# Kernel tuning notes

Measured on AMD Instinct MI355X. Metric: run time of the kernel, lower is better.

The kernel has to match this reference:

```python
import jax, jax.numpy as jnp
import numpy as np

N_NODES = 10000
N_EDGES = 160000
MUL = 128            # channel multiplicity of node features
N_ELEM = 10          # node_attrs scalars (num elements)
N_EDGE_FEATS = 8     # radial basis size
W_NUMEL = 4 * MUL    # 4 uvu paths, 128 weights each
AVG_NEIGH = 16.0
INV_SQRT3 = 0.5773502691896258  # CG coefficient for 1o x 1o -> 0e (dot product path)


def setup_inputs() -> dict:
    key = jax.random.key(0)
    ks = jax.random.split(key, 12)
    node_attrs = jax.random.uniform(ks[0], (N_NODES, N_ELEM), dtype=jnp.float32)
    node_feats = jax.random.normal(ks[1], (N_NODES, MUL * 4), dtype=jnp.float32)  # 128x0e + 128x1o flattened
    edge_attrs = jax.random.normal(ks[2], (N_EDGES, 4), dtype=jnp.float32)        # Y0 (1) + Y1 (3)
    edge_feats = jax.random.normal(ks[3], (N_EDGES, N_EDGE_FEATS), dtype=jnp.float32)
    edge_index = jax.random.randint(ks[4], (2, N_EDGES), 0, N_NODES, dtype=jnp.int64)
    # learned parameters (xavier-ish scales; e3nn path norms folded into weights)
    W_up0 = jax.random.normal(ks[5], (MUL, MUL), dtype=jnp.float32) / np.sqrt(MUL)
    W_up1 = jax.random.normal(ks[6], (MUL, MUL), dtype=jnp.float32) / np.sqrt(MUL)
    W_tpw = jax.random.normal(ks[7], (N_ELEM, N_EDGE_FEATS, W_NUMEL), dtype=jnp.float32) / np.sqrt(N_ELEM * N_EDGE_FEATS)
    W_lin0 = jax.random.normal(ks[8], (2 * MUL, MUL), dtype=jnp.float32) / np.sqrt(2 * MUL)
    W_lin1 = jax.random.normal(ks[9], (2 * MUL, MUL), dtype=jnp.float32) / np.sqrt(2 * MUL)
    W_sk0 = jax.random.normal(ks[10], (MUL, N_ELEM, MUL), dtype=jnp.float32) / np.sqrt(MUL * N_ELEM)
    W_sk1 = jax.random.normal(ks[11], (MUL, N_ELEM, MUL), dtype=jnp.float32) / np.sqrt(MUL * N_ELEM)
    return dict(node_attrs=node_attrs, node_feats=node_feats, edge_attrs=edge_attrs,
                edge_feats=edge_feats, edge_index=edge_index,
                W_up0=W_up0, W_up1=W_up1, W_tpw=W_tpw,
                W_lin0=W_lin0, W_lin1=W_lin1, W_sk0=W_sk0, W_sk1=W_sk1)


def reference(node_attrs, node_feats, edge_attrs, edge_feats, edge_index,
              W_up0, W_up1, W_tpw, W_lin0, W_lin1, W_sk0, W_sk1):
    N = node_feats.shape[0]
    sender, receiver = edge_index[0], edge_index[1]
    x0 = node_feats[:, :MUL]                       # [N,128] scalars (0e)
    x1 = node_feats[:, MUL:].reshape(N, MUL, 3)    # [N,128,3] vectors (1o)

    # skip_tp: FullyConnectedTensorProduct(node_feats, node_attrs -> 128x0e+128x1o)
    sc0 = jnp.einsum('nu,na,uak->nk', x0, node_attrs, W_sk0)        # [N,128]
    sc1 = jnp.einsum('num,na,uak->nkm', x1, node_attrs, W_sk1)      # [N,128,3]

    # linear_up: per-l linear
    h0 = x0 @ W_up0                                   # [N,128]
    h1 = jnp.einsum('num,uk->nkm', x1, W_up1)         # [N,128,3]

    # per-edge TP weights: einsum('be,ba,aek->bk')
    tpw = jnp.einsum('be,ba,aek->bk', edge_feats, node_attrs[sender], W_tpw)  # [E,512]
    w1, w2, w3, w4 = tpw[:, :MUL], tpw[:, MUL:2*MUL], tpw[:, 2*MUL:3*MUL], tpw[:, 3*MUL:]

    Y0 = edge_attrs[:, 0]       # [E]
    Y1 = edge_attrs[:, 1:4]     # [E,3]
    hs0 = h0[sender]            # [E,128] gather
    hs1 = h1[sender]            # [E,128,3]

    # conv_tp (uvu, external per-edge weights), 4 CG paths:
    m0a = w1 * hs0 * Y0[:, None]                                       # 0e x 0e -> 0e
    m1a = (w2 * hs0)[:, :, None] * Y1[:, None, :]                      # 0e x 1o -> 1o
    m1b = hs1 * (w3 * Y0[:, None])[:, :, None]                         # 1o x 0e -> 1o
    m0b = w4 * (INV_SQRT3 * jnp.einsum('eum,em->eu', hs1, Y1))         # 1o x 1o -> 0e
    m0 = jnp.concatenate([m0a, m0b], axis=1)    # [E,256]  irreps_mid 0e block
    m1 = jnp.concatenate([m1a, m1b], axis=1)    # [E,256,3] irreps_mid 1o block

    # scatter_sum over receiver
    msg0 = jax.ops.segment_sum(m0, receiver, num_segments=N)   # [N,256]
    msg1 = jax.ops.segment_sum(m1, receiver, num_segments=N)   # [N,256,3]

    # linear (irreps_mid -> 128x0e+128x1o) / avg_num_neighbors + skip
    out0 = (msg0 @ W_lin0) / AVG_NEIGH + sc0                        # [N,128]
    out1 = jnp.einsum('num,uk->nkm', msg1, W_lin1) / AVG_NEIGH + sc1  # [N,128,3]
    return jnp.concatenate([out0, out1.reshape(N, MUL * 3)], axis=1)  # [N,512]
```

## Files before the change

### kernel.cpp

```cpp
#include <hip/hip_runtime.h>

#define NN 10000
#define NE 160000
#define NBK0 157
#define NBK1 469

constexpr float INV_AVG = 1.0f / 16.0f;
constexpr float INV_SQRT3F = 0.5773502691896258f;

typedef __attribute__((ext_vector_type(8))) short short8v;
typedef __attribute__((ext_vector_type(8))) unsigned short ushort8v;
typedef __attribute__((ext_vector_type(4))) float float4v;

#define OF_UP0 0
#define OF_UP1 16384
#define OF_SK0 32768
#define OF_SK1 196608
#define OF_LN0 360448
#define OF_LN1 393216
#define WPK_TOT 425984
#define WTP_TOT 49152

__device__ __forceinline__ unsigned short f2bf(float f) {
    unsigned int u = __float_as_uint(f);
    return (unsigned short)((u + 0x7FFFu + ((u >> 16) & 1u)) >> 16);
}
__device__ __forceinline__ float bf2f(unsigned short h) {
    return __uint_as_float(((unsigned int)h) << 16);
}

__global__ __launch_bounds__(256) void prep_w_kernel(
    const float* __restrict__ W_up0, const float* __restrict__ W_up1,
    const float* __restrict__ W_sk0, const float* __restrict__ W_sk1,
    const float* __restrict__ W_lin0, const float* __restrict__ W_lin1,
    unsigned short* __restrict__ wpk)
{
    const int g = blockIdx.x * 256 + threadIdx.x;
    if (g >= WPK_TOT / 8) return;
    const float* src; int local, base; bool sk = false;
    if (g < 2048)       { src = W_up0;  local = g;         base = OF_UP0; }
    else if (g < 4096)  { src = W_up1;  local = g - 2048;  base = OF_UP1; }
    else if (g < 24576) { src = W_sk0;  local = g - 4096;  base = OF_SK0; sk = true; }
    else if (g < 45056) { src = W_sk1;  local = g - 24576; base = OF_SK1; sk = true; }
    else if (g < 49152) { src = W_lin0; local = g - 45056; base = OF_LN0; }
    else                { src = W_lin1; local = g - 49152; base = OF_LN1; }
    const int k8 = local >> 7, n = local & 127;
    ushort8v v;
    #pragma unroll
    for (int j = 0; j < 8; ++j) {
        const int k = k8 * 8 + j;
        int row;
        if (sk) { const int a = k >> 7, u = k & 127; row = u * 10 + a; }
        else    { row = k; }
        v[j] = f2bf(src[(size_t)row * 128 + n]);
    }
    *(ushort8v*)(wpk + (size_t)base + (size_t)local * 8) = v;
}

__global__ __launch_bounds__(256) void prep_wt_kernel(
    const float* __restrict__ W_tpw, unsigned short* __restrict__ wtp)
{
    const int g = blockIdx.x * 256 + threadIdx.x;
    if (g >= 6144) return;
    const int k8 = g >> 9, col = g & 511;
    ushort8v v;
    #pragma unroll
    for (int j = 0; j < 8; ++j) {
        const int k = k8 * 8 + j;
        v[j] = (k < 80) ? f2bf(W_tpw[(size_t)k * 512 + col]) : (unsigned short)0;
    }
    *(ushort8v*)(wtp + (size_t)g * 8) = v;
}

__global__ __launch_bounds__(256, 2) void node_mfma_kernel(
    const float* __restrict__ node_attrs,
    const float* __restrict__ node_feats,
    const unsigned short* __restrict__ wpk,
    float* __restrict__ hbuf,
    float* __restrict__ out)
{
    __shared__ __align__(16) unsigned short habuf[1024][8];
    __shared__ __align__(16) unsigned short bbuf[2][1024][8];
    __shared__ float atrow[64][10];

    const int t = threadIdx.x;
    const int bid = blockIdx.x;
    const bool m1 = (bid >= NBK0);
    const int r0 = m1 ? (bid - NBK0) * 64 : bid * 64;
    const int RTOT = m1 ? 30000 : 10000;

    const unsigned short* __restrict__ wup = wpk + (m1 ? OF_UP1 : OF_UP0);
    const unsigned short* __restrict__ wsk = wpk + (m1 ? OF_SK1 : OF_SK0);

    const int rg_ = t >> 2, pg_ = t & 3;
    const int rr_g = min(r0 + rg_, RTOT - 1);
    int n_g, m_g;
    if (!m1) { n_g = rr_g; m_g = 0; }
    else     { n_g = rr_g / 3; m_g = rr_g - n_g * 3; }
    const int wq = rg_ >> 4, rlq = rg_ & 15;

    #pragma unroll
    for (int q = 0; q < 4; ++q) {
        const int sl = pg_ * 4 + q, ss = sl >> 2, kb = sl & 3;
        const int k0 = ss * 32 + kb * 8;
        ushort8v v;
        if (!m1) {
            const float4 xa_ = *(const float4*)(node_feats + (size_t)n_g * 512 + k0);
            const float4 xb_ = *(const float4*)(node_feats + (size_t)n_g * 512 + k0 + 4);
            v[0] = f2bf(xa_.x); v[1] = f2bf(xa_.y); v[2] = f2bf(xa_.z); v[3] = f2bf(xa_.w);
            v[4] = f2bf(xb_.x); v[5] = f2bf(xb_.y); v[6] = f2bf(xb_.z); v[7] = f2bf(xb_.w);
        } else {
            #pragma unroll
            for (int j = 0; j < 8; ++j)
                v[j] = f2bf(node_feats[(size_t)n_g * 512 + 128 + (k0 + j) * 3 + m_g]);
        }
        *(ushort8v*)&habuf[((ss * 4 + wq) * 4 + kb) * 16 + rlq][0] = v;
    }
    for (int i = t; i < 640; i += 256) {
        const int r = i / 10, a = i - r * 10;
        const int rr = min(r0 + r, RTOT - 1);
        const int n = m1 ? (rr / 3) : rr;
        atrow[r][a] = node_attrs[n * 10 + a];
    }
    __syncthreads();

    const int w = t >> 6, lane = t & 63;
    const int rl = lane & 15, kq = lane >> 4;

    {
        float4v hacc[8];
        #pragma unroll
        for (int nt = 0; nt < 8; ++nt) hacc[nt] = (float4v){0.f, 0.f, 0.f, 0.f};

        #pragma unroll
        for (int ss = 0; ss < 4; ++ss) {
            const short8v af = *(const short8v*)&habuf[((ss * 4 + w) * 4 + kq) * 16 + rl][0];
            #pragma unroll
            for (int nt = 0; nt < 8; ++nt) {
                const short8v bf = *(const short8v*)(wup +
                    ((size_t)((ss * 4 + kq) * 128 + nt * 16 + rl)) * 8);
                hacc[nt] = __builtin_amdgcn_mfma_f32_16x16x32_bf16(af, bf, hacc[nt], 0, 0, 0);
            }
        }
        #pragma unroll
        for (int nt = 0; nt < 8; ++nt)
            #pragma unroll
            for (int v2 = 0; v2 < 4; ++v2) {
                const int rr = r0 + w * 16 + kq * 4 + v2;
                if (rr < RTOT) {
                    const int col = nt * 16 + rl;
                    if (!m1) hbuf[(size_t)rr * 512 + col] = hacc[nt][v2];
                    else {
                        const int n = rr / 3, m = rr - n * 3;
                        hbuf[(size_t)n * 512 + 128 + m * 128 + col] = hacc[nt][v2];
                    }
                }
            }
    }

    float4v sacc[8];
    #pragma unroll
    for (int nt = 0; nt < 8; ++nt) sacc[nt] = (float4v){0.f, 0.f, 0.f, 0.f};

    #pragma unroll
    for (int i = 0; i < 4; ++i) {
        const int s = i * 256 + t;
        const int ssb = s >> 9, ntb = (s >> 6) & 7, kbb = (s >> 4) & 3, nlb = s & 15;
        const int k8 = ssb * 4 + kbb;
        const int n = ntb * 16 + nlb;
        *(ushort8v*)&bbuf[0][s][0] =
            *(const ushort8v*)(wsk + ((size_t)(k8 * 128 + n)) * 8);
    }
    __syncthreads();

    int cur = 0;
    for (int ks = 0; ks < 20; ++ks) {
        ushort8v tmp[4];
        if (ks < 19) {
            #pragma unroll
            for (int i = 0; i < 4; ++i) {
                const int s = i * 256 + t;
                const int ssb = s >> 9, ntb = (s >> 6) & 7, kbb = (s >> 4) & 3, nlb = s & 15;
                const int k8 = (ks + 1) * 8 + ssb * 4 + kbb;
                const int n = ntb * 16 + nlb;
                tmp[i] = *(const ushort8v*)(wsk + ((size_t)(k8 * 128 + n)) * 8);
            }
        }

        short8v af[2];
        #pragma unroll
        for (int ss = 0; ss < 2; ++ss) {
            const int kp = ks * 64 + ss * 32 + kq * 8;
            const int a = kp >> 7, u0 = kp & 127;
            const ushort8v xh = *(const ushort8v*)&habuf[
                (((u0 >> 5) * 4 + w) * 4 + ((u0 >> 3) & 3)) * 16 + rl][0];
            const float av = atrow[w * 16 + rl][a];
            ushort8v vv;
            #pragma unroll
            for (int j = 0; j < 8; ++j) vv[j] = f2bf(bf2f(xh[j]) * av);
            af[ss] = (short8v)vv;
        }

        #pragma unroll
        for (int ss = 0; ss < 2; ++ss)
            #pragma unroll
            for (int nt = 0; nt < 8; ++nt) {
                const short8v bf =
                    *(const short8v*)&bbuf[cur][((ss * 8 + nt) * 4 + kq) * 16 + rl][0];
                sacc[nt] = __builtin_amdgcn_mfma_f32_16x16x32_bf16(af[ss], bf, sacc[nt], 0, 0, 0);
            }

        if (ks < 19) {
            #pragma unroll
            for (int i = 0; i < 4; ++i) {
                const int s = i * 256 + t;
                *(ushort8v*)&bbuf[cur ^ 1][s][0] = tmp[i];
            }
        }
        __syncthreads();
        cur ^= 1;
    }

    #pragma unroll
    for (int nt = 0; nt < 8; ++nt)
        #pragma unroll
        for (int v2 = 0; v2 < 4; ++v2) {
            const int rr = r0 + w * 16 + kq * 4 + v2;
            if (rr < RTOT) {
                const int col = nt * 16 + rl;
                if (!m1) out[(size_t)rr * 512 + col] = sacc[nt][v2];
                else {
                    const int n = rr / 3, m = rr - n * 3;
                    out[(size_t)n * 512 + 128 + col * 3 + m] = sacc[nt][v2];
                }
            }
        }
}

__global__ __launch_bounds__(256) void hist_kernel(
    const int* __restrict__ recv, int* __restrict__ cnt)
{
    const int e = blockIdx.x * 256 + threadIdx.x;
    if (e < NE) atomicAdd(&cnt[recv[e]], 1);
}

__global__ __launch_bounds__(256) void scan_kernel(
    const int* __restrict__ cnt, int* __restrict__ row_start,
    int* __restrict__ head)
{
    __shared__ int part[256];
    const int t = threadIdx.x;
    const int base = t * 40;
    int s = 0;
    if (base < NN)
        for (int b = 0; b < 40; ++b) s += cnt[base + b];
    part[t] = s;
    __syncthreads();
    const int local = s;
    for (int off = 1; off < 256; off <<= 1) {
        const int v = (t >= off) ? part[t - off] : 0;
        __syncthreads();
        part[t] += v;
        __syncthreads();
    }
    const int excl = part[t] - local;
    if (base < NN) {
        int run = excl;
        for (int b = 0; b < 40; ++b) {
            row_start[base + b] = run;
            head[base + b] = run;
            run += cnt[base + b];
        }
    }
    if (t == 0) row_start[NN] = NE;
}

__global__ __launch_bounds__(256) void scatter_kernel(
    const int* __restrict__ recv, int* __restrict__ head,
    int* __restrict__ elist)
{
    const int e = blockIdx.x * 256 + threadIdx.x;
    if (e < NE) {
        const int p = atomicAdd(&head[recv[e]], 1);
        elist[p] = e;
    }
}

__global__ __launch_bounds__(256) void pack2_kernel(
    const float* __restrict__ node_attrs,
    const float* __restrict__ edge_attrs,
    const float* __restrict__ edge_feats,
    const int*  __restrict__ edge_index,
    const int*  __restrict__ elist,
    unsigned short* __restrict__ zpk,
    float* __restrict__ ypk)
{
    const int pos = blockIdx.x * 256 + threadIdx.x;
    if (pos >= NE) return;
    const int e = elist[pos];
    const int snd = edge_index[e];

    float ef[8];
    *(float4*)&ef[0] = *(const float4*)(edge_feats + (size_t)e * 8);
    *(float4*)&ef[4] = *(const float4*)(edge_feats + (size_t)e * 8 + 4);
    float at[10];
    #pragma unroll
    for (int a = 0; a < 10; ++a) at[a] = node_attrs[(size_t)snd * 10 + a];

    #pragma unroll
    for (int k8 = 0; k8 < 12; ++k8) {
        ushort8v v;
        #pragma unroll
        for (int j = 0; j < 8; ++j) {
            const int A = k8 * 8 + j;
            const float z = (A < 80) ? at[A >> 3] * ef[A & 7] : 0.f;
            v[j] = f2bf(z);
        }
        *(ushort8v*)(zpk + ((size_t)k8 * NE + pos) * 8) = v;
    }

    const float4 ea = *(const float4*)(edge_attrs + (size_t)e * 4);
    *(float4*)(ypk + (size_t)pos * 8) = ea;
    *(float4*)(ypk + (size_t)pos * 8 + 4) =
        make_float4(__int_as_float(snd), 0.f, 0.f, 0.f);
}

__global__ __launch_bounds__(512, 2) void gather_mfma_kernel(
    const unsigned short* __restrict__ wtp,
    const float* __restrict__ hbuf,
    const int*  __restrict__ row_start,
    const unsigned short* __restrict__ zpk,
    const float* __restrict__ ypk,
    float* __restrict__ msgbuf)
{
    __shared__ __align__(16) unsigned short zb[384][8];
    __shared__ float yb[32][9];

    const int t = threadIdx.x;
    const int ngrp = blockIdx.x;
    const int w8 = t >> 6, lane = t & 63;
    const int p = w8 >> 2;
    const int w = w8 & 3;
    const int rl = lane & 15, kq = lane >> 4;

    short8v breg[2][3][2];
    #pragma unroll
    for (int wi = 0; wi < 2; ++wi)
        #pragma unroll
        for (int ks = 0; ks < 3; ++ks)
            #pragma unroll
            for (int ct = 0; ct < 2; ++ct) {
                const int col = p * 256 + wi * 128 + w * 32 + ct * 16 + rl;
                breg[wi][ks][ct] = *(const short8v*)(wtp +
                    ((size_t)((ks * 4 + kq) * 512 + col)) * 8);
            }

    for (int nn = 0; nn < 4; ++nn) {
        const int node = ngrp * 4 + nn;
        const int rowst = row_start[node];
        const int deg = row_start[node + 1] - rowst;

        float nacc[2][4];
        #pragma unroll
        for (int ct = 0; ct < 2; ++ct)
            #pragma unroll
            for (int j = 0; j < 4; ++j) nacc[ct][j] = 0.f;

        for (int ce = 0; ce < deg; ce += 32) {
            const int cl = min(32, deg - ce);
            __syncthreads();

            if (t < 384) {
                const int s = t;
                const int rl2 = s & 15, kq2 = (s >> 4) & 3;
                const int rowt2 = (s >> 6) & 1, ks2 = s >> 7;
                const int e = rowt2 * 16 + rl2;
                const int k8 = ks2 * 4 + kq2;
                ushort8v v = {0, 0, 0, 0, 0, 0, 0, 0};
                if (e < cl)
                    v = *(const ushort8v*)(zpk + ((size_t)k8 * NE + rowst + ce + e) * 8);
                *(ushort8v*)&zb[s][0] = v;
            }
            else if (t >= 448) {
                const int tt = t - 448;
                const int row = tt >> 1, half = tt & 1;
                float4 v = make_float4(0.f, 0.f, 0.f, 0.f);
                if (row < cl)
                    v = *(const float4*)(ypk + (size_t)(rowst + ce + row) * 8 + half * 4);
                yb[row][half * 4 + 0] = v.x;
                yb[row][half * 4 + 1] = v.y;
                yb[row][half * 4 + 2] = v.z;
                yb[row][half * 4 + 3] = v.w;
            }
            __syncthreads();

            if (p == 0) {
                #pragma unroll
                for (int rt = 0; rt < 2; ++rt) {
                    if (rt == 1 && cl <= 16) continue;
                    float h0v[4][2];
                    #pragma unroll
                    for (int v = 0; v < 4; ++v) {
                        const int e = rt * 16 + kq * 4 + v;
                        const int snd = __float_as_int(yb[e][4]);
                        const float* hrow = hbuf + (size_t)snd * 512;
                        #pragma unroll
                        for (int ct = 0; ct < 2; ++ct)
                            h0v[v][ct] = hrow[w * 32 + ct * 16 + rl];
                    }
                    float4v acc[2][2];
                    #pragma unroll
                    for (int wi = 0; wi < 2; ++wi)
                        #pragma unroll
                        for (int ct = 0; ct < 2; ++ct)
                            acc[wi][ct] = (float4v){0.f, 0.f, 0.f, 0.f};
                    #pragma unroll
                    for (int ks = 0; ks < 3; ++ks) {
                        const short8v af =
                            *(const short8v*)&zb[ks * 128 + rt * 64 + lane][0];
                        #pragma unroll
                        for (int wi = 0; wi < 2; ++wi)
                            #pragma unroll
                            for (int ct = 0; ct < 2; ++ct)
                                acc[wi][ct] = __builtin_amdgcn_mfma_f32_16x16x32_bf16(
                                    af, breg[wi][ks][ct], acc[wi][ct], 0, 0, 0);
                    }
                    #pragma unroll
                    for (int v = 0; v < 4; ++v) {
                        const int e = rt * 16 + kq * 4 + v;
                        const float Y0  = yb[e][0];
                        const float Y10 = yb[e][1];
                        const float Y11 = yb[e][2];
                        const float Y12 = yb[e][3];
                        #pragma unroll
                        for (int ct = 0; ct < 2; ++ct) {
                            const float tA = acc[0][ct][v];
                            const float tB = acc[1][ct][v];
                            const float h0 = h0v[v][ct];
                            nacc[ct][0] = fmaf(tA * Y0, h0, nacc[ct][0]);
                            const float tm = tB * h0;
                            nacc[ct][1] = fmaf(tm, Y10, nacc[ct][1]);
                            nacc[ct][2] = fmaf(tm, Y11, nacc[ct][2]);
                            nacc[ct][3] = fmaf(tm, Y12, nacc[ct][3]);
                        }
                    }
                }
            } else {
                #pragma unroll
                for (int rt = 0; rt < 2; ++rt) {
                    if (rt == 1 && cl <= 16) continue;
                    float hA[4][2], hB[4][2], hC[4][2];
                    #pragma unroll
                    for (int v = 0; v < 4; ++v) {
                        const int e = rt * 16 + kq * 4 + v;
                        const int snd = __float_as_int(yb[e][4]);
                        const float* hrow = hbuf + (size_t)snd * 512;
                        #pragma unroll
                        for (int ct = 0; ct < 2; ++ct) {
                            const int c = w * 32 + ct * 16 + rl;
                            hA[v][ct] = hrow[128 + c];
                            hB[v][ct] = hrow[256 + c];
                            hC[v][ct] = hrow[384 + c];
                        }
                    }
                    float4v acc[2][2];
                    #pragma unroll
                    for (int wi = 0; wi < 2; ++wi)
                        #pragma unroll
                        for (int ct = 0; ct < 2; ++ct)
                            acc[wi][ct] = (float4v){0.f, 0.f, 0.f, 0.f};
                    #pragma unroll
                    for (int ks = 0; ks < 3; ++ks) {
                        const short8v af =
                            *(const short8v*)&zb[ks * 128 + rt * 64 + lane][0];
                        #pragma unroll
                        for (int wi = 0; wi < 2; ++wi)
                            #pragma unroll
                            for (int ct = 0; ct < 2; ++ct)
                                acc[wi][ct] = __builtin_amdgcn_mfma_f32_16x16x32_bf16(
                                    af, breg[wi][ks][ct], acc[wi][ct], 0, 0, 0);
                    }
                    #pragma unroll
                    for (int v = 0; v < 4; ++v) {
                        const int e = rt * 16 + kq * 4 + v;
                        const float Y0  = yb[e][0];
                        const float Y10 = yb[e][1];
                        const float Y11 = yb[e][2];
                        const float Y12 = yb[e][3];
                        #pragma unroll
                        for (int ct = 0; ct < 2; ++ct) {
                            const float tA = acc[0][ct][v];
                            const float tB = acc[1][ct][v];
                            const float t2 = tA * Y0;
                            nacc[ct][1] = fmaf(t2, hA[v][ct], nacc[ct][1]);
                            nacc[ct][2] = fmaf(t2, hB[v][ct], nacc[ct][2]);
                            nacc[ct][3] = fmaf(t2, hC[v][ct], nacc[ct][3]);
                            float d = hA[v][ct] * Y10;
                            d = fmaf(hB[v][ct], Y11, d);
                            d = fmaf(hC[v][ct], Y12, d);
                            nacc[ct][0] = fmaf(tB * INV_SQRT3F, d, nacc[ct][0]);
                        }
                    }
                }
            }
        }

        float red[2][4];
        #pragma unroll
        for (int ct = 0; ct < 2; ++ct)
            #pragma unroll
            for (int j = 0; j < 4; ++j) {
                float v = nacc[ct][j];
                v += __shfl_xor(v, 16, 64);
                v += __shfl_xor(v, 32, 64);
                red[ct][j] = v;
            }
        if (kq == 0) {
            float* mrow = msgbuf + (size_t)node * 1024;
            #pragma unroll
            for (int ct = 0; ct < 2; ++ct) {
                const int c = w * 32 + ct * 16 + rl;
                if (p == 0) {
                    mrow[c]       = red[ct][0];
                    mrow[256 + c] = red[ct][1];
                    mrow[512 + c] = red[ct][2];
                    mrow[768 + c] = red[ct][3];
                } else {
                    mrow[128 + c] = red[ct][0];
                    mrow[384 + c] = red[ct][1];
                    mrow[640 + c] = red[ct][2];
                    mrow[896 + c] = red[ct][3];
                }
            }
        }
    }
}

__global__ __launch_bounds__(256, 2) void out_mfma_kernel(
    const float* __restrict__ msgbuf,
    const unsigned short* __restrict__ wpk,
    float* __restrict__ out)
{
    __shared__ __align__(16) unsigned short habuf[2048][8];

    const int t = threadIdx.x;
    const int n0 = blockIdx.x * 16;

    const int rg_ = t >> 2, pg_ = t & 3;
    const int wq = rg_ >> 4, rlq = rg_ & 15;
    const float* src = msgbuf + (size_t)(n0 + rlq) * 1024 + wq * 256;

    #pragma unroll
    for (int q = 0; q < 8; ++q) {
        const int sl = pg_ * 8 + q, ss = sl >> 2, kb = sl & 3;
        const int k0 = ss * 32 + kb * 8;
        const float4 xa = *(const float4*)(src + k0);
        const float4 xb = *(const float4*)(src + k0 + 4);
        ushort8v v;
        v[0] = f2bf(xa.x); v[1] = f2bf(xa.y); v[2] = f2bf(xa.z); v[3] = f2bf(xa.w);
        v[4] = f2bf(xb.x); v[5] = f2bf(xb.y); v[6] = f2bf(xb.z); v[7] = f2bf(xb.w);
        *(ushort8v*)&habuf[((ss * 4 + wq) * 4 + kb) * 16 + rlq][0] = v;
    }
    __syncthreads();

    const int w = t >> 6, lane = t & 63;
    const int rl = lane & 15, kq = lane >> 4;
    const unsigned short* __restrict__ wl = wpk + ((w == 0) ? OF_LN0 : OF_LN1);

    float4v acc[8];
    #pragma unroll
    for (int nt = 0; nt < 8; ++nt) acc[nt] = (float4v){0.f, 0.f, 0.f, 0.f};

    #pragma unroll
    for (int ss = 0; ss < 8; ++ss) {
        const short8v af = *(const short8v*)&habuf[((ss * 4 + w) * 4 + kq) * 16 + rl][0];
        #pragma unroll
        for (int nt = 0; nt < 8; ++nt) {
            const short8v bf = *(const short8v*)(wl +
                ((size_t)((ss * 4 + kq) * 128 + nt * 16 + rl)) * 8);
            acc[nt] = __builtin_amdgcn_mfma_f32_16x16x32_bf16(af, bf, acc[nt], 0, 0, 0);
        }
    }

    #pragma unroll
    for (int nt = 0; nt < 8; ++nt)
        #pragma unroll
        for (int v2 = 0; v2 < 4; ++v2) {
            const int n = n0 + kq * 4 + v2;
            const int col = nt * 16 + rl;
            if (w == 0) {
                out[(size_t)n * 512 + col] += acc[nt][v2] * INV_AVG;
            } else {
                const int m = w - 1;
                out[(size_t)n * 512 + 128 + col * 3 + m] += acc[nt][v2] * INV_AVG;
            }
        }
}

extern "C" void kernel_launch(void* const* d_in, const int* in_sizes, int n_in,
                              void* d_out, int out_size, void* d_ws, size_t ws_size,
                              hipStream_t stream) {
    const float* node_attrs = (const float*)d_in[0];
    const float* node_feats = (const float*)d_in[1];
    const float* edge_attrs = (const float*)d_in[2];
    const float* edge_feats = (const float*)d_in[3];
    const int*   edge_index = (const int*)d_in[4];
    const float* W_up0  = (const float*)d_in[5];
    const float* W_up1  = (const float*)d_in[6];
    const float* W_tpw  = (const float*)d_in[7];
    const float* W_lin0 = (const float*)d_in[8];
    const float* W_lin1 = (const float*)d_in[9];
    const float* W_sk0  = (const float*)d_in[10];
    const float* W_sk1  = (const float*)d_in[11];
    float* out = (float*)d_out;

    float* hbuf   = (float*)d_ws;
    float* msgbuf = hbuf + (size_t)NN * 512;
    float* ypk    = msgbuf + (size_t)NN * 1024;
    unsigned short* zpk = (unsigned short*)(ypk + (size_t)NE * 8);
    unsigned short* wpk = zpk + (size_t)12 * NE * 8;
    unsigned short* wtp = wpk + WPK_TOT;
    int* cnt       = (int*)(wtp + WTP_TOT);
    int* row_start = cnt + NN;
    int* head      = row_start + NN + 1;
    int* elist     = head + NN;

    const int* recv = edge_index + NE;

    hipMemsetAsync(cnt, 0, NN * sizeof(int), stream);
    hist_kernel<<<(NE + 255) / 256, 256, 0, stream>>>(recv, cnt);
    scan_kernel<<<1, 256, 0, stream>>>(cnt, row_start, head);
    scatter_kernel<<<(NE + 255) / 256, 256, 0, stream>>>(recv, head, elist);
    pack2_kernel<<<(NE + 255) / 256, 256, 0, stream>>>(
        node_attrs, edge_attrs, edge_feats, edge_index, elist, zpk, ypk);
    prep_w_kernel<<<(WPK_TOT / 8 + 255) / 256, 256, 0, stream>>>(
        W_up0, W_up1, W_sk0, W_sk1, W_lin0, W_lin1, wpk);
    prep_wt_kernel<<<24, 256, 0, stream>>>(W_tpw, wtp);

    node_mfma_kernel<<<NBK0 + NBK1, 256, 0, stream>>>(node_attrs, node_feats,
                                                      wpk, hbuf, out);
    gather_mfma_kernel<<<2500, 512, 0, stream>>>(wtp, hbuf, row_start,
                                                 zpk, ypk, msgbuf);
    out_mfma_kernel<<<NN / 16, 256, 0, stream>>>(msgbuf, wpk, out);
}
```

Measured before the change: 217.4 us.

## Split gather kernel into per-half blocks and drop LDS staging barriers

The 512-thread gather block, which staged edge tiles in shared memory behind two __syncthreads per chunk, becomes two 256-thread blocks per node group, one for the scalar half and one for the vector half. Each wave now loads its MFMA A-fragments, sender indices and spherical harmonics directly from global memory into registers. This removes the barriers and shared-memory round trips and lets the two halves schedule independently. In exchange, both blocks and all four waves reload the same z, y and sender data from global memory, which relies on L2/L1 caching to absorb the redundant traffic.

```diff
diff --git a/kernel.cpp b/kernel.cpp
--- a/kernel.cpp
+++ b/kernel.cpp
@@ -325,7 +325,7 @@
         make_float4(__int_as_float(snd), 0.f, 0.f, 0.f);
 }
 
-__global__ __launch_bounds__(512, 2) void gather_mfma_kernel(
+__global__ __launch_bounds__(256, 2) void gather_mfma_kernel(
     const unsigned short* __restrict__ wtp,
     const float* __restrict__ hbuf,
     const int*  __restrict__ row_start,
@@ -333,14 +333,10 @@
     const float* __restrict__ ypk,
     float* __restrict__ msgbuf)
 {
-    __shared__ __align__(16) unsigned short zb[384][8];
-    __shared__ float yb[32][9];
-
     const int t = threadIdx.x;
-    const int ngrp = blockIdx.x;
-    const int w8 = t >> 6, lane = t & 63;
-    const int p = w8 >> 2;
-    const int w = w8 & 3;
+    const int p = blockIdx.x & 1;
+    const int ngrp = blockIdx.x >> 1;
+    const int w = t >> 6, lane = t & 63;
     const int rl = lane & 15, kq = lane >> 4;
 
     short8v breg[2][3][2];
@@ -368,70 +364,85 @@
 
         for (int ce = 0; ce < deg; ce += 32) {
             const int cl = min(32, deg - ce);
-            __syncthreads();
-
-            if (t < 384) {
-                const int s = t;
-                const int rl2 = s & 15, kq2 = (s >> 4) & 3;
-                const int rowt2 = (s >> 6) & 1, ks2 = s >> 7;
-                const int e = rowt2 * 16 + rl2;
-                const int k8 = ks2 * 4 + kq2;
-                ushort8v v = {0, 0, 0, 0, 0, 0, 0, 0};
-                if (e < cl)
-                    v = *(const ushort8v*)(zpk + ((size_t)k8 * NE + rowst + ce + e) * 8);
-                *(ushort8v*)&zb[s][0] = v;
-            }
-            else if (t >= 448) {
-                const int tt = t - 448;
-                const int row = tt >> 1, half = tt & 1;
-                float4 v = make_float4(0.f, 0.f, 0.f, 0.f);
-                if (row < cl)
-                    v = *(const float4*)(ypk + (size_t)(rowst + ce + row) * 8 + half * 4);
-                yb[row][half * 4 + 0] = v.x;
-                yb[row][half * 4 + 1] = v.y;
-                yb[row][half * 4 + 2] = v.z;
-                yb[row][half * 4 + 3] = v.w;
-            }
-            __syncthreads();
-
-            if (p == 0) {
+
+            #pragma unroll
+            for (int rt = 0; rt < 2; ++rt) {
+                if (rt == 1 && cl <= 16) continue;
+
+                int snd[4];
                 #pragma unroll
-                for (int rt = 0; rt < 2; ++rt) {
-                    if (rt == 1 && cl <= 16) continue;
-                    float h0v[4][2];
+                for (int v = 0; v < 4; ++v) {
+                    const int e = rt * 16 + kq * 4 + v;
+                    snd[v] = (e < cl)
+                        ? __float_as_int(ypk[(size_t)(rowst + ce + e) * 8 + 4]) : 0;
+                }
+
+                float h0v[4][2];
+                float hA[4][2], hB[4][2], hC[4][2];
+                if (p == 0) {
                     #pragma unroll
                     for (int v = 0; v < 4; ++v) {
-                        const int e = rt * 16 + kq * 4 + v;
-                        const int snd = __float_as_int(yb[e][4]);
-                        const float* hrow = hbuf + (size_t)snd * 512;
+                        const float* hrow = hbuf + (size_t)snd[v] * 512;
                         #pragma unroll
                         for (int ct = 0; ct < 2; ++ct)
                             h0v[v][ct] = hrow[w * 32 + ct * 16 + rl];
                     }
-                    float4v acc[2][2];
+                } else {
+                    #pragma unroll
+                    for (int v = 0; v < 4; ++v) {
+                        const float* hrow = hbuf + (size_t)snd[v] * 512;
+                        #pragma unroll
+                        for (int ct = 0; ct < 2; ++ct) {
+                            const int c = w * 32 + ct * 16 + rl;
+                            hA[v][ct] = hrow[128 + c];
+                            hB[v][ct] = hrow[256 + c];
+                            hC[v][ct] = hrow[384 + c];
+                        }
+                    }
+                }
+
+                short8v af[3];
+                {
+                    const int e = rt * 16 + rl;
+                    #pragma unroll
+                    for (int ks = 0; ks < 3; ++ks) {
+                        ushort8v vz = {0, 0, 0, 0, 0, 0, 0, 0};
+                        if (e < cl)
+                            vz = *(const ushort8v*)(zpk +
+                                ((size_t)(ks * 4 + kq) * NE + rowst + ce + e) * 8);
+                        af[ks] = (short8v)vz;
+                    }
+                }
+
+                float4v acc[2][2];
+                #pragma unroll
+                for (int wi = 0; wi < 2; ++wi)
+                    #pragma unroll
+                    for (int ct = 0; ct < 2; ++ct)
+                        acc[wi][ct] = (float4v){0.f, 0.f, 0.f, 0.f};
+                #pragma unroll
+                for (int ks = 0; ks < 3; ++ks)
                     #pragma unroll
                     for (int wi = 0; wi < 2; ++wi)
                         #pragma unroll
                         for (int ct = 0; ct < 2; ++ct)
-                            acc[wi][ct] = (float4v){0.f, 0.f, 0.f, 0.f};
-                    #pragma unroll
-                    for (int ks = 0; ks < 3; ++ks) {
-                        const short8v af =
-                            *(const short8v*)&zb[ks * 128 + rt * 64 + lane][0];
-                        #pragma unroll
-                        for (int wi = 0; wi < 2; ++wi)
-                            #pragma unroll
-                            for (int ct = 0; ct < 2; ++ct)
-                                acc[wi][ct] = __builtin_amdgcn_mfma_f32_16x16x32_bf16(
-                                    af, breg[wi][ks][ct], acc[wi][ct], 0, 0, 0);
-                    }
+                            acc[wi][ct] = __builtin_amdgcn_mfma_f32_16x16x32_bf16(
+                                af[ks], breg[wi][ks][ct], acc[wi][ct], 0, 0, 0);
+
+                float4 yv[4];
+                #pragma unroll
+                for (int v = 0; v < 4; ++v) {
+                    const int e = rt * 16 + kq * 4 + v;
+                    yv[v] = (e < cl)
+                        ? *(const float4*)(ypk + (size_t)(rowst + ce + e) * 8)
+                        : make_float4(0.f, 0.f, 0.f, 0.f);
+                }
+
+                if (p == 0) {
                     #pragma unroll
                     for (int v = 0; v < 4; ++v) {
-                        const int e = rt * 16 + kq * 4 + v;
-                        const float Y0  = yb[e][0];
-                        const float Y10 = yb[e][1];
-                        const float Y11 = yb[e][2];
-                        const float Y12 = yb[e][3];
+                        const float Y0 = yv[v].x, Y10 = yv[v].y;
+                        const float Y11 = yv[v].z, Y12 = yv[v].w;
                         #pragma unroll
                         for (int ct = 0; ct < 2; ++ct) {
                             const float tA = acc[0][ct][v];
@@ -444,49 +455,11 @@
                             nacc[ct][3] = fmaf(tm, Y12, nacc[ct][3]);
                         }
                     }
-                }
-            } else {
-                #pragma unroll
-                for (int rt = 0; rt < 2; ++rt) {
-                    if (rt == 1 && cl <= 16) continue;
-                    float hA[4][2], hB[4][2], hC[4][2];
+                } else {
                     #pragma unroll
                     for (int v = 0; v < 4; ++v) {
-                        const int e = rt * 16 + kq * 4 + v;
-                        const int snd = __float_as_int(yb[e][4]);
-                        const float* hrow = hbuf + (size_t)snd * 512;
-                        #pragma unroll
-                        for (int ct = 0; ct < 2; ++ct) {
-                            const int c = w * 32 + ct * 16 + rl;
-                            hA[v][ct] = hrow[128 + c];
-                            hB[v][ct] = hrow[256 + c];
-                            hC[v][ct] = hrow[384 + c];
-                        }
-                    }
-                    float4v acc[2][2];
-                    #pragma unroll
-                    for (int wi = 0; wi < 2; ++wi)
-                        #pragma unroll
-                        for (int ct = 0; ct < 2; ++ct)
-                            acc[wi][ct] = (float4v){0.f, 0.f, 0.f, 0.f};
-                    #pragma unroll
-                    for (int ks = 0; ks < 3; ++ks) {
-                        const short8v af =
-                            *(const short8v*)&zb[ks * 128 + rt * 64 + lane][0];
-                        #pragma unroll
-                        for (int wi = 0; wi < 2; ++wi)
-                            #pragma unroll
-                            for (int ct = 0; ct < 2; ++ct)
-                                acc[wi][ct] = __builtin_amdgcn_mfma_f32_16x16x32_bf16(
-                                    af, breg[wi][ks][ct], acc[wi][ct], 0, 0, 0);
-                    }
-                    #pragma unroll
-                    for (int v = 0; v < 4; ++v) {
-                        const int e = rt * 16 + kq * 4 + v;
-                        const float Y0  = yb[e][0];
-                        const float Y10 = yb[e][1];
-                        const float Y11 = yb[e][2];
-                        const float Y12 = yb[e][3];
+                        const float Y0 = yv[v].x, Y10 = yv[v].y;
+                        const float Y11 = yv[v].z, Y12 = yv[v].w;
                         #pragma unroll
                         for (int ct = 0; ct < 2; ++ct) {
                             const float tA = acc[0][ct][v];
@@ -639,7 +612,7 @@
 
     node_mfma_kernel<<<NBK0 + NBK1, 256, 0, stream>>>(node_attrs, node_feats,
                                                       wpk, hbuf, out);
-    gather_mfma_kernel<<<2500, 512, 0, stream>>>(wtp, hbuf, row_start,
+    gather_mfma_kernel<<<5000, 256, 0, stream>>>(wtp, hbuf, row_start,
                                                  zpk, ypk, msgbuf);
     out_mfma_kernel<<<NN / 16, 256, 0, stream>>>(msgbuf, wpk, out);
 }
```

After: 286.5 us. 31.8% more time.
